# Performance work log

Hardware: AMD Instinct MI355X
Metric: run time of the kernel (lower is better)

Reference implementation:

```python
import jax, jax.numpy as jnp
import numpy as np

NUM_NODES = 25
EMBED_DIM = 64
OUT_SIZE = 2
N_TOTAL = 204800   # 8192 graphs * 25 nodes
N_EDGES = 3276800  # avg degree 16


def setup_inputs() -> dict:
    key = jax.random.key(0)
    ks = jax.random.split(key, 8)
    x = jax.random.normal(ks[0], (N_TOTAL, EMBED_DIM), dtype=jnp.float32)
    # random edges; real graphs are graph-local but math is identical
    edge_index = jax.random.randint(ks[1], (2, N_EDGES), 0, N_TOTAL, dtype=jnp.int32)
    batch = jnp.repeat(jnp.arange(N_TOTAL // NUM_NODES, dtype=jnp.int32), NUM_NODES)
    hid = NUM_NODES * EMBED_DIM  # 1600
    W_conv = jax.random.normal(ks[2], (EMBED_DIM, EMBED_DIM), dtype=jnp.float32) / np.sqrt(EMBED_DIM)
    b_conv = jnp.zeros((EMBED_DIM,), dtype=jnp.float32)
    W1 = jax.random.normal(ks[3], (hid, hid), dtype=jnp.float32) / np.sqrt(hid)
    b1 = jnp.zeros((hid,), dtype=jnp.float32)
    W2 = jax.random.normal(ks[4], (hid, OUT_SIZE), dtype=jnp.float32) / np.sqrt(hid)
    b2 = jnp.zeros((OUT_SIZE,), dtype=jnp.float32)
    return {"x": x, "edge_index": edge_index, "batch": batch,
            "W_conv": W_conv, "b_conv": b_conv,
            "W1": W1, "b1": b1, "W2": W2, "b2": b2}


def reference(x, edge_index, batch, W_conv, b_conv, W1, b1, W2, b2):
    N = x.shape[0]
    # --- GCNConv: add self-loops, symmetric degree norm, transform, scatter-add ---
    loop = jnp.arange(N, dtype=edge_index.dtype)
    src = jnp.concatenate([edge_index[0], loop])
    dst = jnp.concatenate([edge_index[1], loop])
    deg = jax.ops.segment_sum(jnp.ones_like(dst, dtype=x.dtype), dst, num_segments=N)
    dinv = jax.lax.rsqrt(deg)  # deg >= 1 due to self-loops
    norm = dinv[src] * dinv[dst]                       # [E+N]
    h = x @ W_conv                                     # [N, D]
    msg = h[src] * norm[:, None]                       # gather + scale
    h = jax.ops.segment_sum(msg, dst, num_segments=N) + b_conv
    h = jax.nn.relu(h)
    # --- dense head ---
    nb = -(-batch.shape[0] // NUM_NODES)               # ceil
    h = h.reshape(nb, NUM_NODES * EMBED_DIM)           # [B, 1600]
    h = jax.nn.relu(h @ W1 + b1)
    logits = h @ W2 + b2
    return jax.nn.softmax(logits, axis=-1)
```

## Files before the change

kernel.cpp:

```cpp
#include <hip/hip_runtime.h>
#include <hip/hip_bf16.h>
#include <stdint.h>

#define NT   204800
#define NE   3276800
#define ED   64
#define NBG  8192
#define HID  1600
#define CAP  56
#define NBKT 400
#define BCAP 9216

typedef float  f32x4  __attribute__((ext_vector_type(4)));
typedef __bf16 bf16x8 __attribute__((ext_vector_type(8)));

__device__ __forceinline__ void async_ld16(const void* g, void* l) {
    __builtin_amdgcn_global_load_lds(
        (__attribute__((address_space(1))) const void*)g,
        (__attribute__((address_space(3))) void*)l, 16, 0, 0);
}

__device__ __forceinline__ unsigned short f2bf_raw(float f) {
    __hip_bfloat16 h = __float2bfloat16(f);
    return *(unsigned short*)&h;
}

__global__ void k_initg(int* __restrict__ gcur) {
    int t = threadIdx.x;
    if (t < NBKT) gcur[t] = t * BCAP;
}

__global__ __launch_bounds__(256) void k_part(const int* __restrict__ srcv,
                                              const int* __restrict__ dstv,
                                              int* __restrict__ gcur,
                                              unsigned* __restrict__ rec) {
    __shared__ int hist[NBKT];
    __shared__ int gofs[NBKT];
    const int t = threadIdx.x;
    const int base = blockIdx.x * (NE / 512);
    for (int i = t; i < NBKT; i += 256) hist[i] = 0;
    __syncthreads();
    unsigned keep[25];
#pragma unroll
    for (int j = 0; j < 25; ++j) {
        int d = dstv[base + j * 256 + t];
        int b = d >> 9;
        int ls = atomicAdd(&hist[b], 1);
        keep[j] = ((unsigned)ls << 18) | ((unsigned)(d & 511) << 9) | (unsigned)b;
    }
    __syncthreads();
    for (int i = t; i < NBKT; i += 256) gofs[i] = atomicAdd(&gcur[i], hist[i]);
    __syncthreads();
#pragma unroll
    for (int j = 0; j < 25; ++j) {
        int s = srcv[base + j * 256 + t];
        unsigned k = keep[j];
        int b   = (int)(k & 511u);
        int rel = (int)((k >> 9) & 511u);
        int idx = gofs[b] + (int)(k >> 18);
        if (idx < (b + 1) * BCAP)
            rec[idx] = ((unsigned)s << 9) | (unsigned)rel;
    }
}

__global__ __launch_bounds__(512) void k_fillb(const int* __restrict__ gcur,
                                               const unsigned* __restrict__ rec,
                                               int* __restrict__ cur,
                                               int* __restrict__ csr,
                                               float* __restrict__ dinv) {
    __shared__ int cnt[512];
    const int t = threadIdx.x;
    const int b = blockIdx.x;
    const int n0 = b * 512;
    cnt[t] = 0;
    __syncthreads();
    const int bstart = b * BCAP;
    int bcnt = gcur[b] - bstart;
    bcnt = (bcnt > BCAP) ? BCAP : bcnt;
    for (int idx = t; idx < bcnt; idx += 512) {
        unsigned r = rec[bstart + idx];
        unsigned rel = r & 511u;
        int ls = atomicAdd(&cnt[rel], 1);
        if (ls < CAP) csr[(size_t)(n0 + rel) * CAP + ls] = (int)(r >> 9);
    }
    __syncthreads();
    int cn = cnt[t];
    cur[n0 + t] = cn;
    dinv[n0 + t] = rsqrtf((float)cn + 1.f);
}

__global__ __launch_bounds__(256) void k_gemm_conv(const float* __restrict__ x,
                                                   const float* __restrict__ Wc,
                                                   const float* __restrict__ dinv,
                                                   __hip_bfloat16* __restrict__ hbs) {
    __shared__ unsigned short Xs[64 * 72];
    __shared__ unsigned short Wt[64 * 72];
    const int t = threadIdx.x;
    const int row0 = blockIdx.x * 64;
#pragma unroll
    for (int i = 0; i < 4; ++i) {
        int idx = i * 256 + t;
        int r = idx >> 4, c4 = (idx & 15) << 2;
        f32x4 wv = ((const f32x4*)Wc)[idx];
        Wt[(c4 + 0) * 72 + r] = f2bf_raw(wv.x);
        Wt[(c4 + 1) * 72 + r] = f2bf_raw(wv.y);
        Wt[(c4 + 2) * 72 + r] = f2bf_raw(wv.z);
        Wt[(c4 + 3) * 72 + r] = f2bf_raw(wv.w);
        f32x4 xv = ((const f32x4*)(x + (size_t)row0 * 64))[idx];
        ushort4 p;
        p.x = f2bf_raw(xv.x);
        p.y = f2bf_raw(xv.y);
        p.z = f2bf_raw(xv.z);
        p.w = f2bf_raw(xv.w);
        *(ushort4*)&Xs[r * 72 + c4] = p;
    }
    __syncthreads();
    const int w = t >> 6, lane = t & 63;
    const int fr = lane & 15, fq = lane >> 4;
    f32x4 acc[4] = {};
#pragma unroll
    for (int kb = 0; kb < 2; ++kb) {
        bf16x8 av = *(const bf16x8*)&Xs[(w * 16 + fr) * 72 + kb * 32 + fq * 8];
#pragma unroll
        for (int j = 0; j < 4; ++j) {
            bf16x8 bv = *(const bf16x8*)&Wt[(j * 16 + fr) * 72 + kb * 32 + fq * 8];
            acc[j] = __builtin_amdgcn_mfma_f32_16x16x32_bf16(av, bv, acc[j], 0, 0, 0);
        }
    }
#pragma unroll
    for (int r = 0; r < 4; ++r) {
        int row = row0 + w * 16 + fq * 4 + r;
        float di = dinv[row];
        unsigned short* dst = (unsigned short*)&hbs[(size_t)row * 64];
#pragma unroll
        for (int j = 0; j < 4; ++j)
            dst[j * 16 + fr] = f2bf_raw(acc[j][r] * di);
    }
}

__global__ __launch_bounds__(256) void k_gather(const int* __restrict__ cur,
                                                const int* __restrict__ csr,
                                                const float* __restrict__ dinv,
                                                const __hip_bfloat16* __restrict__ hbs,
                                                const float* __restrict__ bc,
                                                __hip_bfloat16* __restrict__ Hb) {
    const int lane = threadIdx.x & 63;
    const int du = __builtin_amdgcn_readfirstlane(blockIdx.x * 4 + (threadIdx.x >> 6));
    const float di = dinv[du];
    int cn = cur[du];
    cn = (cn > CAP) ? CAP : cn;
    const int* __restrict__ lst = csr + (size_t)du * CAP;
    const float self = __bfloat162float(hbs[(size_t)du * ED + lane]);
    float acc = self;
    int e = 0;
    for (; e + 16 <= cn; e += 16) {
#pragma unroll
        for (int q = 0; q < 16; ++q) {
            int s = lst[e + q];
            acc += __bfloat162float(hbs[(size_t)s * ED + lane]);
        }
    }
    if (e < cn) {
        const int pad = e + 16 - cn;
#pragma unroll
        for (int q = 0; q < 16; ++q) {
            int s = (e + q < cn) ? lst[e + q] : du;
            acc += __bfloat162float(hbs[(size_t)s * ED + lane]);
        }
        acc = fmaf(-(float)pad, self, acc);
    }
    Hb[(size_t)du * ED + lane] = __float2bfloat16(fmaxf(bc[lane] + di * acc, 0.f));
}

__global__ void k_convW1(const float* __restrict__ W1, __hip_bfloat16* __restrict__ Bt) {
    __shared__ float tile[64][65];
    const int t = threadIdx.x;
    const int k0 = blockIdx.x * 64;
    const int n0 = blockIdx.y * 64;
#pragma unroll
    for (int i = 0; i < 16; ++i) {
        int lin = i * 256 + t;
        int r = lin >> 6, c = lin & 63;
        tile[r][c] = W1[(size_t)(k0 + r) * HID + n0 + c];
    }
    __syncthreads();
#pragma unroll
    for (int i = 0; i < 16; ++i) {
        int lin = i * 256 + t;
        int nn = lin >> 6, kk = lin & 63;
        Bt[(size_t)(n0 + nn) * HID + k0 + kk] = __float2bfloat16(tile[kk][nn]);
    }
}

__global__ __launch_bounds__(256) void k_gemm1(const __hip_bfloat16* __restrict__ A,
                                               const __hip_bfloat16* __restrict__ Bt,
                                               const float* __restrict__ b1,
                                               __hip_bfloat16* __restrict__ h2) {
    __shared__ unsigned short As[2][128 * 32];
    __shared__ unsigned short Bs[2][64 * 32];
    const int t = threadIdx.x;
    const int lane = t & 63;
    const int wave = t >> 6;
    const int lin = blockIdx.y * 64 + blockIdx.x;
    const int xc  = lin & 7;
    const int pos = lin >> 3;
    const int bm0 = (xc * 8 + (pos & 7)) * 128;
    const int bn0 = (pos >> 3) * 64;
    const int wm = (wave >> 1) * 64;
    const int wn = (wave & 1) * 32;
    const int fr = lane & 15;
    const int fq = lane >> 4;
    const int sr = t >> 2;
    const int scs = (((t & 3) ^ ((sr >> 1) & 3)) * 8);
    const __hip_bfloat16* ga0 = A + (size_t)(bm0 + sr) * HID + scs;
    const __hip_bfloat16* ga1 = A + (size_t)(bm0 + 64 + sr) * HID + scs;
    const __hip_bfloat16* gb0 = Bt + (size_t)(bn0 + sr) * HID + scs;
    const int rdx = (fr >> 1) & 3;
    const int fao = (wm + fr) * 32 + (fq ^ rdx) * 8;
    const int fbo = (wn + fr) * 32 + (fq ^ rdx) * 8;
    f32x4 acc[4][2] = {};

#define STAGE(bidx) do { \
        unsigned short* dA_ = &As[bidx][0]; unsigned short* dB_ = &Bs[bidx][0]; \
        async_ld16(ga0, dA_ + t * 8);  async_ld16(ga1, dA_ + (256 + t) * 8); \
        async_ld16(gb0, dB_ + t * 8); \
        ga0 += 32; ga1 += 32; gb0 += 32; } while (0)

    const int NKT = HID / 32;
    STAGE(0);
    STAGE(1);
#pragma unroll 2
    for (int kt = 0; kt < NKT; ++kt) {
        const int p = kt & 1;
        if (kt < NKT - 1)
            asm volatile("s_waitcnt vmcnt(3)\n\ts_barrier" ::: "memory");
        else
            asm volatile("s_waitcnt vmcnt(0)\n\ts_barrier" ::: "memory");
        const unsigned short* fa = &As[p][fao];
        const unsigned short* fb = &Bs[p][fbo];
        bf16x8 av[4], bv[2];
#pragma unroll
        for (int i = 0; i < 4; ++i) av[i] = *(const bf16x8*)(fa + i * 16 * 32);
#pragma unroll
        for (int j = 0; j < 2; ++j) bv[j] = *(const bf16x8*)(fb + j * 16 * 32);
#pragma unroll
        for (int i = 0; i < 4; ++i)
#pragma unroll
            for (int j = 0; j < 2; ++j)
                acc[i][j] = __builtin_amdgcn_mfma_f32_16x16x32_bf16(av[i], bv[j], acc[i][j], 0, 0, 0);
        if (kt < NKT - 2) {
            asm volatile("s_waitcnt lgkmcnt(0)\n\ts_barrier" ::: "memory");
            STAGE(p);
        }
    }
#undef STAGE

#pragma unroll
    for (int j = 0; j < 2; ++j) {
        int n = bn0 + wn + j * 16 + fr;
        float bias = b1[n];
#pragma unroll
        for (int i = 0; i < 4; ++i) {
#pragma unroll
            for (int r = 0; r < 4; ++r) {
                int m = bm0 + wm + i * 16 + fq * 4 + r;
                float v = acc[i][j][r] + bias;
                h2[(size_t)m * HID + n] = __float2bfloat16(fmaxf(v, 0.f));
            }
        }
    }
}

__global__ void k_head(const __hip_bfloat16* __restrict__ h2, const float* __restrict__ W2,
                       const float* __restrict__ b2, float* __restrict__ out) {
    int g = blockIdx.x * 4 + (threadIdx.x >> 6);
    int lane = threadIdx.x & 63;
    const __hip_bfloat16* row = h2 + (size_t)g * HID;
    float a0 = 0.f, a1 = 0.f;
#pragma unroll
    for (int i = 0; i < 25; ++i) {
        int k = i * 64 + lane;
        float hv = __bfloat162float(row[k]);
        float2 w = ((const float2*)W2)[k];
        a0 += hv * w.x;
        a1 += hv * w.y;
    }
#pragma unroll
    for (int off = 32; off > 0; off >>= 1) {
        a0 += __shfl_down(a0, off, 64);
        a1 += __shfl_down(a1, off, 64);
    }
    if (lane == 0) {
        float l0 = a0 + b2[0], l1 = a1 + b2[1];
        float mx = fmaxf(l0, l1);
        float e0 = expf(l0 - mx), e1 = expf(l1 - mx);
        float s = e0 + e1;
        out[2 * g]     = e0 / s;
        out[2 * g + 1] = e1 / s;
    }
}

extern "C" void kernel_launch(void* const* d_in, const int* in_sizes, int n_in,
                              void* d_out, int out_size, void* d_ws, size_t ws_size,
                              hipStream_t stream) {
    const float* x  = (const float*)d_in[0];
    const int*   ei = (const int*)d_in[1];
    const float* Wc = (const float*)d_in[3];
    const float* bc = (const float*)d_in[4];
    const float* W1 = (const float*)d_in[5];
    const float* b1 = (const float*)d_in[6];
    const float* W2 = (const float*)d_in[7];
    const float* b2 = (const float*)d_in[8];
    float* out = (float*)d_out;

    const int* srcv = ei;
    const int* dstv = ei + NE;

    char* ws = (char*)d_ws;
    int*   cur  = (int*)ws;
    float* dinv = (float*)(ws + 819200);
    int*   gcur = (int*)(ws + 1638400);
    int*   csr  = (int*)(ws + 1642496);
    unsigned* rec = (unsigned*)(ws + 47517696);
    __hip_bfloat16* hbs = (__hip_bfloat16*)(ws + 47517696);
    __hip_bfloat16* h2  = (__hip_bfloat16*)(ws + 47517696);
    __hip_bfloat16* Hb  = (__hip_bfloat16*)(ws + 73732096);
    __hip_bfloat16* Bt  = (__hip_bfloat16*)(ws + 99946496);

    k_initg    <<<1, 512, 0, stream>>>(gcur);
    k_part     <<<512, 256, 0, stream>>>(srcv, dstv, gcur, rec);
    k_fillb    <<<NBKT, 512, 0, stream>>>(gcur, rec, cur, csr, dinv);
    k_gemm_conv<<<NT / 64, 256, 0, stream>>>(x, Wc, dinv, hbs);
    k_gather   <<<NT / 4, 256, 0, stream>>>(cur, csr, dinv, hbs, bc, Hb);
    k_convW1   <<<dim3(HID / 64, HID / 64), 256, 0, stream>>>(W1, Bt);
    k_gemm1    <<<dim3(NBG / 128, HID / 64), 256, 0, stream>>>(Hb, Bt, b1, h2);
    k_head     <<<NBG / 4, 256, 0, stream>>>(h2, W2, b2, out);
}
```

Measured before the change: 376.1 us.

## Restructure GEMM1 to 2 waves with 64x64 per-wave tiles and BK=64

The 8192x1600x1600 GEMM block now runs 128 threads (2 waves) instead of 4. Each wave computes a 64x64 output tile with 16 accumulators, and the K-step doubles to 64 with a new XOR swizzle for LDS. The aim is more MFMA work per LDS fragment load and half as many barriers and K iterations. The cost is higher register pressure, lower occupancy per block and a 1D grid of 1600 blocks with the block-index remapping changed.

Result: no change. 377.6 us (+0.4%).

```diff
diff --git a/kernel.cpp b/kernel.cpp
--- a/kernel.cpp
+++ b/kernel.cpp
@@ -192,78 +192,89 @@
     }
 }
 
-__global__ __launch_bounds__(256) void k_gemm1(const __hip_bfloat16* __restrict__ A,
+__global__ __launch_bounds__(128) void k_gemm1(const __hip_bfloat16* __restrict__ A,
                                                const __hip_bfloat16* __restrict__ Bt,
                                                const float* __restrict__ b1,
                                                __hip_bfloat16* __restrict__ h2) {
-    __shared__ unsigned short As[2][128 * 32];
-    __shared__ unsigned short Bs[2][64 * 32];
+    __shared__ unsigned short As[2][128 * 64];
+    __shared__ unsigned short Bs[2][64 * 64];
     const int t = threadIdx.x;
     const int lane = t & 63;
-    const int wave = t >> 6;
-    const int lin = blockIdx.y * 64 + blockIdx.x;
+    const int w = t >> 6;
+    const int lin = blockIdx.x;
     const int xc  = lin & 7;
     const int pos = lin >> 3;
     const int bm0 = (xc * 8 + (pos & 7)) * 128;
     const int bn0 = (pos >> 3) * 64;
-    const int wm = (wave >> 1) * 64;
-    const int wn = (wave & 1) * 32;
     const int fr = lane & 15;
     const int fq = lane >> 4;
-    const int sr = t >> 2;
-    const int scs = (((t & 3) ^ ((sr >> 1) & 3)) * 8);
-    const __hip_bfloat16* ga0 = A + (size_t)(bm0 + sr) * HID + scs;
-    const __hip_bfloat16* ga1 = A + (size_t)(bm0 + 64 + sr) * HID + scs;
-    const __hip_bfloat16* gb0 = Bt + (size_t)(bn0 + sr) * HID + scs;
-    const int rdx = (fr >> 1) & 3;
-    const int fao = (wm + fr) * 32 + (fq ^ rdx) * 8;
-    const int fbo = (wn + fr) * 32 + (fq ^ rdx) * 8;
-    f32x4 acc[4][2] = {};
-
-#define STAGE(bidx) do { \
-        unsigned short* dA_ = &As[bidx][0]; unsigned short* dB_ = &Bs[bidx][0]; \
-        async_ld16(ga0, dA_ + t * 8);  async_ld16(ga1, dA_ + (256 + t) * 8); \
-        async_ld16(gb0, dB_ + t * 8); \
-        ga0 += 32; ga1 += 32; gb0 += 32; } while (0)
-
-    const int NKT = HID / 32;
+    const int lrow  = lane >> 3;
+    const int lslot = (lane & 7) ^ lrow;
+    const size_t soff = (size_t)lrow * HID + lslot * 8;
+    const __hip_bfloat16* pa = A  + (size_t)bm0 * HID + soff;
+    const __hip_bfloat16* pb = Bt + (size_t)bn0 * HID + soff;
+    const int ra  = (w * 64 + fr) * 64;
+    const int rb  = fr * 64;
+    const int sl0 = ((0 + fq) ^ (fr & 7)) * 8;
+    const int sl1 = ((4 + fq) ^ (fr & 7)) * 8;
+    f32x4 acc[4][4] = {};
+
+    auto STAGE = [&](int bidx) {
+        unsigned short* dA = &As[bidx][(w * 8) * 512 + lane * 8];
+        const __hip_bfloat16* sA = pa + (size_t)(w * 8) * 8 * HID;
+#pragma unroll
+        for (int q = 0; q < 8; ++q)
+            async_ld16(sA + (size_t)q * 8 * HID, dA + q * 512);
+        unsigned short* dB = &Bs[bidx][(w * 4) * 512 + lane * 8];
+        const __hip_bfloat16* sB = pb + (size_t)(w * 4) * 8 * HID;
+#pragma unroll
+        for (int q = 0; q < 4; ++q)
+            async_ld16(sB + (size_t)q * 8 * HID, dB + q * 512);
+        pa += 64; pb += 64;
+    };
+
+    const int NKT = HID / 64;
     STAGE(0);
     STAGE(1);
-#pragma unroll 2
     for (int kt = 0; kt < NKT; ++kt) {
         const int p = kt & 1;
         if (kt < NKT - 1)
-            asm volatile("s_waitcnt vmcnt(3)\n\ts_barrier" ::: "memory");
+            asm volatile("s_waitcnt vmcnt(12)\n\ts_barrier" ::: "memory");
         else
             asm volatile("s_waitcnt vmcnt(0)\n\ts_barrier" ::: "memory");
-        const unsigned short* fa = &As[p][fao];
-        const unsigned short* fb = &Bs[p][fbo];
-        bf16x8 av[4], bv[2];
-#pragma unroll
-        for (int i = 0; i < 4; ++i) av[i] = *(const bf16x8*)(fa + i * 16 * 32);
-#pragma unroll
-        for (int j = 0; j < 2; ++j) bv[j] = *(const bf16x8*)(fb + j * 16 * 32);
+        bf16x8 av0[4], av1[4], bv0[4], bv1[4];
+#pragma unroll
+        for (int i = 0; i < 4; ++i) {
+            av0[i] = *(const bf16x8*)&As[p][ra + i * 16 * 64 + sl0];
+            av1[i] = *(const bf16x8*)&As[p][ra + i * 16 * 64 + sl1];
+        }
+#pragma unroll
+        for (int j = 0; j < 4; ++j) {
+            bv0[j] = *(const bf16x8*)&Bs[p][rb + j * 16 * 64 + sl0];
+            bv1[j] = *(const bf16x8*)&Bs[p][rb + j * 16 * 64 + sl1];
+        }
 #pragma unroll
         for (int i = 0; i < 4; ++i)
 #pragma unroll
-            for (int j = 0; j < 2; ++j)
-                acc[i][j] = __builtin_amdgcn_mfma_f32_16x16x32_bf16(av[i], bv[j], acc[i][j], 0, 0, 0);
+            for (int j = 0; j < 4; ++j) {
+                acc[i][j] = __builtin_amdgcn_mfma_f32_16x16x32_bf16(av0[i], bv0[j], acc[i][j], 0, 0, 0);
+                acc[i][j] = __builtin_amdgcn_mfma_f32_16x16x32_bf16(av1[i], bv1[j], acc[i][j], 0, 0, 0);
+            }
         if (kt < NKT - 2) {
             asm volatile("s_waitcnt lgkmcnt(0)\n\ts_barrier" ::: "memory");
             STAGE(p);
         }
     }
-#undef STAGE
-
-#pragma unroll
-    for (int j = 0; j < 2; ++j) {
-        int n = bn0 + wn + j * 16 + fr;
+
+#pragma unroll
+    for (int j = 0; j < 4; ++j) {
+        int n = bn0 + j * 16 + fr;
         float bias = b1[n];
 #pragma unroll
         for (int i = 0; i < 4; ++i) {
 #pragma unroll
             for (int r = 0; r < 4; ++r) {
-                int m = bm0 + wm + i * 16 + fq * 4 + r;
+                int m = bm0 + w * 64 + i * 16 + fq * 4 + r;
                 float v = acc[i][j][r] + bias;
                 h2[(size_t)m * HID + n] = __float2bfloat16(fmaxf(v, 0.f));
             }
@@ -333,6 +344,6 @@
     k_gemm_conv<<<NT / 64, 256, 0, stream>>>(x, Wc, dinv, hbs);
     k_gather   <<<NT / 4, 256, 0, stream>>>(cur, csr, dinv, hbs, bc, Hb);
     k_convW1   <<<dim3(HID / 64, HID / 64), 256, 0, stream>>>(W1, Bt);
-    k_gemm1    <<<dim3(NBG / 128, HID / 64), 256, 0, stream>>>(Hb, Bt, b1, h2);
+    k_gemm1    <<<1600, 128, 0, stream>>>(Hb, Bt, b1, h2);
     k_head     <<<NBG / 4, 256, 0, stream>>>(h2, W2, b2, out);
 }
```
